# Kernel optimization log

Hardware: AMD Instinct MI355X
Metric: run time of the kernel (lower is better)

The kernel has to match this reference:

```python
import jax, jax.numpy as jnp
import numpy as np
import math

DIM = 768
HEADS = 8
DIM_HEAD = 64
INNER = HEADS * DIM_HEAD  # 512
B, L = 2, 4096
LN_EPS = 1e-5


def setup_inputs() -> dict:
    key = jax.random.key(0)
    ks = jax.random.split(key, 6)
    std = 0.02
    return {
        "x": jax.random.normal(ks[0], (B, L, DIM), dtype=jnp.float32),
        "ln_gamma": jnp.ones((DIM,), dtype=jnp.float32),
        "ln_beta": jnp.zeros((DIM,), dtype=jnp.float32),
        "Wq": jax.random.normal(ks[1], (DIM, INNER), dtype=jnp.float32) * std,
        "Wkv": jax.random.normal(ks[2], (DIM, 2 * INNER), dtype=jnp.float32) * std,
        "Wo": jax.random.normal(ks[3], (INNER, DIM), dtype=jnp.float32) * std,
    }


def reference(x, ln_gamma, ln_beta, Wq, Wkv, Wo):
    b, l, _ = x.shape
    # LayerNorm (eps=1e-5, affine)
    mu = jnp.mean(x, axis=-1, keepdims=True)
    var = jnp.mean(jnp.square(x - mu), axis=-1, keepdims=True)
    xn = (x - mu) * jax.lax.rsqrt(var + LN_EPS) * ln_gamma + ln_beta

    q = xn @ Wq                      # (b, l, inner)
    kv = xn @ Wkv                    # (b, l, 2*inner)
    k, v = jnp.split(kv, 2, axis=-1)

    def to_heads(t):
        return t.reshape(b, l, HEADS, DIM_HEAD).transpose(0, 2, 1, 3)  # (b,h,l,d)

    q, k, v = to_heads(q), to_heads(k), to_heads(v)

    scale = 1.0 / math.sqrt(math.sqrt(DIM_HEAD))
    # explicit quadratic scores, softmax in float32 as in original
    weight = jnp.einsum("bhid,bhjd->bhij", q * scale, k * scale)
    weight = jax.nn.softmax(weight.astype(jnp.float32), axis=-1).astype(q.dtype)
    out = jnp.einsum("bhij,bhjd->bhid", weight, v)       # (b,h,l,d)
    out = out.transpose(0, 2, 1, 3).reshape(b, l, INNER)  # merge heads
    return out @ Wo
```

## Files before the change

kernel.cpp:

```cpp
#include <hip/hip_runtime.h>
#include <hip/hip_bf16.h>


typedef __bf16 bf16_t;
typedef __bf16 bf16x4 __attribute__((ext_vector_type(4)));
typedef __bf16 bf16x8 __attribute__((ext_vector_type(8)));
typedef float f32x4 __attribute__((ext_vector_type(4)));

#define MFMA16(a, b, c) __builtin_amdgcn_mfma_f32_16x16x32_bf16((a), (b), (c), 0, 0, 0)

#define QSCALE 0.18033688011112042f

#define GLDS(gp, lp)                                                          \
    __builtin_amdgcn_global_load_lds(                                         \
        (const __attribute__((address_space(1))) void*)(gp),                  \
        (__attribute__((address_space(3))) void*)(lp), 16, 0, 0)

__global__ void detect_kernel(const unsigned int* __restrict__ xw, int* __restrict__ flag) {
    const int i = threadIdx.x;
    int cnt = 0;
#pragma unroll
    for (int j = 0; j < 2; ++j) {
        const unsigned int e = (xw[i * 2 + j] >> 7) & 0xFF;
        cnt += (e >= 100 && e <= 140) ? 1 : 0;
    }
#pragma unroll
    for (int off = 1; off < 64; off <<= 1) cnt += __shfl_xor(cnt, off, 64);
    if (i == 0) *flag = (cnt < 64) ? 1 : 0;
}

__global__ __launch_bounds__(256) void ln_kernel(const void* __restrict__ xv,
                                                 const void* __restrict__ gv,
                                                 const void* __restrict__ bv,
                                                 bf16_t* __restrict__ xn,
                                                 const int* __restrict__ flag) {
    const int f32 = *flag;
    const int lane = threadIdx.x & 63;
    const int row = blockIdx.x * 4 + (threadIdx.x >> 6);
    const int c0 = lane * 12;

    float v[12];
    if (f32) {
        const float* xr = (const float*)xv + (size_t)row * 768 + c0;
#pragma unroll
        for (int i = 0; i < 3; ++i) {
            const float4 q = *(const float4*)(xr + i * 4);
            v[i * 4] = q.x; v[i * 4 + 1] = q.y; v[i * 4 + 2] = q.z; v[i * 4 + 3] = q.w;
        }
    } else {
        const bf16_t* xr = (const bf16_t*)xv + (size_t)row * 768 + c0;
#pragma unroll
        for (int i = 0; i < 3; ++i) {
            const bf16x4 q = *(const bf16x4*)(xr + i * 4);
#pragma unroll
            for (int j = 0; j < 4; ++j) v[i * 4 + j] = (float)q[j];
        }
    }
    float s = 0.f, sq = 0.f;
#pragma unroll
    for (int j = 0; j < 12; ++j) { s += v[j]; sq += v[j] * v[j]; }
#pragma unroll
    for (int off = 1; off < 64; off <<= 1) {
        s += __shfl_xor(s, off, 64);
        sq += __shfl_xor(sq, off, 64);
    }
    const float mu = s * (1.0f / 768.0f);
    const float var = sq * (1.0f / 768.0f) - mu * mu;
    const float rstd = rsqrtf(var + 1e-5f);

    bf16_t* xo = xn + (size_t)row * 768 + c0;
#pragma unroll
    for (int i = 0; i < 3; ++i) {
        bf16x4 o;
#pragma unroll
        for (int j = 0; j < 4; ++j) {
            const int c = c0 + i * 4 + j;
            const float gc = f32 ? ((const float*)gv)[c] : (float)((const bf16_t*)gv)[c];
            const float bc = f32 ? ((const float*)bv)[c] : (float)((const bf16_t*)bv)[c];
            o[j] = (bf16_t)((v[i * 4 + j] - mu) * rstd * gc + bc);
        }
        *(bf16x4*)(xo + i * 4) = o;
    }
}

__global__ __launch_bounds__(256) void transpose_w(const void* __restrict__ in,
                                                   bf16_t* __restrict__ out,
                                                   int R, int C,
                                                   const int* __restrict__ flag) {
    const int f32 = *flag;
    __shared__ bf16_t Ts[64 * 68];
    const int r0 = blockIdx.y * 64, c0 = blockIdx.x * 64;
    const int t = threadIdx.x;
    {
        const int r = t >> 2, c = (t & 3) * 16;
        if (f32) {
            const float* src = (const float*)in + (size_t)(r0 + r) * C + c0 + c;
#pragma unroll
            for (int i = 0; i < 16; i += 4) {
                const float4 q = *(const float4*)(src + i);
                Ts[r * 68 + c + i] = (bf16_t)q.x;
                Ts[r * 68 + c + i + 1] = (bf16_t)q.y;
                Ts[r * 68 + c + i + 2] = (bf16_t)q.z;
                Ts[r * 68 + c + i + 3] = (bf16_t)q.w;
            }
        } else {
            const bf16_t* src = (const bf16_t*)in + (size_t)(r0 + r) * C + c0 + c;
            *(bf16x8*)&Ts[r * 68 + c] = *(const bf16x8*)src;
            *(bf16x8*)&Ts[r * 68 + c + 8] = *(const bf16x8*)(src + 8);
        }
    }
    __syncthreads();
    {
        const int oc = t >> 2, seg = (t & 3) * 16;
        bf16x8 v0, v1;
#pragma unroll
        for (int j = 0; j < 8; ++j) v0[j] = Ts[(seg + j) * 68 + oc];
#pragma unroll
        for (int j = 0; j < 8; ++j) v1[j] = Ts[(seg + 8 + j) * 68 + oc];
        bf16_t* dst = out + (size_t)(c0 + oc) * R + r0 + seg;
        *(bf16x8*)dst = v0;
        *(bf16x8*)(dst + 8) = v1;
    }
}

__global__ __launch_bounds__(256) void gemm_bt(const bf16_t* __restrict__ A,
                                               const bf16_t* __restrict__ BT,
                                               void* __restrict__ C,
                                               int M, int N, int K,
                                               const int* __restrict__ out_flag) {
    const int m0 = blockIdx.y * 128;
    const int n0 = blockIdx.x * 128;
    __shared__ bf16_t As[128 * 32];
    __shared__ bf16_t Bs[128 * 32];

    const int t = threadIdx.x;
    const int lane = t & 63;
    const int w = t >> 6;
    const int wm = (w >> 1) * 64;
    const int wn = (w & 1) * 64;
    const int quad = lane >> 4;
    const int cl = lane & 15;

    f32x4 acc[4][4];
    const f32x4 z4 = {0.f, 0.f, 0.f, 0.f};
#pragma unroll
    for (int mi = 0; mi < 4; ++mi)
#pragma unroll
        for (int ni = 0; ni < 4; ++ni) acc[mi][ni] = z4;

    const int r0 = lane >> 2;
    const int c0 = (lane & 3) * 8;
    const bf16_t* AgL = A + (size_t)(m0 + w * 32 + r0) * K + c0;
    const bf16_t* AgH = A + (size_t)(m0 + w * 32 + 16 + r0) * K + c0;
    const bf16_t* BgL = BT + (size_t)(n0 + w * 32 + r0) * K + c0;
    const bf16_t* BgH = BT + (size_t)(n0 + w * 32 + 16 + r0) * K + c0;
    bf16_t* AdL = &As[(w * 32) * 32];
    bf16_t* AdH = &As[(w * 32 + 16) * 32];
    bf16_t* BdL = &Bs[(w * 32) * 32];
    bf16_t* BdH = &Bs[(w * 32 + 16) * 32];

    for (int kt = 0; kt < K; kt += 32) {
        __syncthreads();
        GLDS(AgL + kt, AdL);
        GLDS(AgH + kt, AdH);
        GLDS(BgL + kt, BdL);
        GLDS(BgH + kt, BdH);
        __syncthreads();

        const int ko = quad * 8;
        bf16x8 af[4], bfr[4];
#pragma unroll
        for (int mi = 0; mi < 4; ++mi)
            af[mi] = *(const bf16x8*)&As[(wm + mi * 16 + cl) * 32 + ko];
#pragma unroll
        for (int ni = 0; ni < 4; ++ni)
            bfr[ni] = *(const bf16x8*)&Bs[(wn + ni * 16 + cl) * 32 + ko];
#pragma unroll
        for (int mi = 0; mi < 4; ++mi)
#pragma unroll
            for (int ni = 0; ni < 4; ++ni)
                acc[mi][ni] = MFMA16(af[mi], bfr[ni], acc[mi][ni]);
    }

    const int f32out = (out_flag != nullptr) && (*out_flag != 0);
#pragma unroll
    for (int mi = 0; mi < 4; ++mi) {
#pragma unroll
        for (int ni = 0; ni < 4; ++ni) {
#pragma unroll
            for (int r4 = 0; r4 < 4; ++r4) {
                const int row = m0 + wm + mi * 16 + quad * 4 + r4;
                const int col = n0 + wn + ni * 16 + cl;
                if (f32out)
                    ((float*)C)[(size_t)row * N + col] = acc[mi][ni][r4];
                else
                    ((bf16_t*)C)[(size_t)row * N + col] = (bf16_t)acc[mi][ni][r4];
            }
        }
    }
}

__global__ __launch_bounds__(128) void gemm_bt64(const bf16_t* __restrict__ A,
                                                 const bf16_t* __restrict__ BT,
                                                 void* __restrict__ C,
                                                 int M, int N, int K,
                                                 const int* __restrict__ out_flag) {
    const int m0 = blockIdx.y * 128;
    const int n0 = blockIdx.x * 64;
    __shared__ bf16_t As[128 * 32];
    __shared__ bf16_t Bs[64 * 32];

    const int t = threadIdx.x;
    const int lane = t & 63;
    const int w = t >> 6;
    const int quad = lane >> 4;
    const int cl = lane & 15;

    f32x4 acc[4][4];
    const f32x4 z4 = {0.f, 0.f, 0.f, 0.f};
#pragma unroll
    for (int mi = 0; mi < 4; ++mi)
#pragma unroll
        for (int ni = 0; ni < 4; ++ni) acc[mi][ni] = z4;

    const int r0 = lane >> 2;
    const int c0 = (lane & 3) * 8;
    const bf16_t* Ag = A + (size_t)(m0 + w * 64 + r0) * K + c0;
    const bf16_t* Bg = BT + (size_t)(n0 + w * 32 + r0) * K + c0;
    bf16_t* Ad = &As[(w * 64) * 32];
    bf16_t* Bd = &Bs[(w * 32) * 32];

    for (int kt = 0; kt < K; kt += 32) {
        __syncthreads();
#pragma unroll
        for (int i = 0; i < 4; ++i) GLDS(Ag + kt + (size_t)i * 16 * K, Ad + i * 512);
#pragma unroll
        for (int i = 0; i < 2; ++i) GLDS(Bg + kt + (size_t)i * 16 * K, Bd + i * 512);
        __syncthreads();

        const int ko = quad * 8;
        bf16x8 af[4], bfr[4];
#pragma unroll
        for (int mi = 0; mi < 4; ++mi)
            af[mi] = *(const bf16x8*)&As[(w * 64 + mi * 16 + cl) * 32 + ko];
#pragma unroll
        for (int ni = 0; ni < 4; ++ni)
            bfr[ni] = *(const bf16x8*)&Bs[(ni * 16 + cl) * 32 + ko];
#pragma unroll
        for (int mi = 0; mi < 4; ++mi)
#pragma unroll
            for (int ni = 0; ni < 4; ++ni)
                acc[mi][ni] = MFMA16(af[mi], bfr[ni], acc[mi][ni]);
    }

    const int f32out = (out_flag != nullptr) && (*out_flag != 0);
#pragma unroll
    for (int mi = 0; mi < 4; ++mi) {
#pragma unroll
        for (int ni = 0; ni < 4; ++ni) {
#pragma unroll
            for (int r4 = 0; r4 < 4; ++r4) {
                const int row = m0 + w * 64 + mi * 16 + quad * 4 + r4;
                const int col = n0 + ni * 16 + cl;
                if (f32out)
                    ((float*)C)[(size_t)row * N + col] = acc[mi][ni][r4];
                else
                    ((bf16_t*)C)[(size_t)row * N + col] = (bf16_t)acc[mi][ni][r4];
            }
        }
    }
}

__global__ __launch_bounds__(256) void vtrans(const bf16_t* __restrict__ qkv,
                                              bf16_t* __restrict__ vtg) {
    const int tt = blockIdx.x;
    const int bh = blockIdx.y;
    const int b = bh >> 3, h = bh & 7;
    const int tok0 = tt * 64;
    __shared__ bf16_t Ts[64 * 68];
    const int t = threadIdx.x;
    {
        const int r = t >> 2, c = (t & 3) * 16;
        const bf16_t* src = qkv + ((size_t)b * 4096 + tok0 + r) * 1536 + 1024 + h * 64 + c;
        *(bf16x8*)&Ts[r * 68 + c] = *(const bf16x8*)src;
        *(bf16x8*)&Ts[r * 68 + c + 8] = *(const bf16x8*)(src + 8);
    }
    __syncthreads();
    {
        const int d = t >> 2, seg = (t & 3) * 16;
        bf16x8 v0, v1;
#pragma unroll
        for (int j = 0; j < 8; ++j) v0[j] = Ts[(seg + j) * 68 + d];
#pragma unroll
        for (int j = 0; j < 8; ++j) v1[j] = Ts[(seg + 8 + j) * 68 + d];
        bf16_t* dst = vtg + ((size_t)bh * 64 + d) * 4096 + tok0 + seg;
        *(bf16x8*)dst = v0;
        *(bf16x8*)(dst + 8) = v1;
    }
}

__global__ __launch_bounds__(256, 2) void attn_kernel(const bf16_t* __restrict__ qkv,
                                                      const bf16_t* __restrict__ vtg,
                                                      bf16_t* __restrict__ ao) {
    const int qt = blockIdx.x;
    const int bh = blockIdx.y;
    const int b = bh >> 3, h = bh & 7;
    const int q0 = qt * 128;

    __shared__ bf16_t Ps[4][64 * 68];
    __shared__ bf16_t Ks[2][64 * 68];
    __shared__ bf16_t Vs[2][64 * 68];

    const int t = threadIdx.x;
    const int lane = t & 63;
    const int w = t >> 6;
    const int qsub = w & 1;
    const int kh = w >> 1;
    const int quad = lane >> 4;
    const int cl = lane & 15;

    const size_t rowbase = (size_t)b * 4096;
    const int qcol = h * 64;
    const int kcol = 512 + h * 64;

    {
        const int r = t >> 1;
        const int half = (t & 1) * 32;
        const bf16_t* src = qkv + (rowbase + q0 + r) * 1536 + qcol + half;
#pragma unroll
        for (int o8 = 0; o8 < 4; ++o8) {
            bf16x8 v = *(const bf16x8*)(src + o8 * 8);
#pragma unroll
            for (int e = 0; e < 8; ++e) v[e] = (bf16_t)((float)v[e] * QSCALE);
            *(bf16x8*)&Ps[0][r * 68 + half + o8 * 8] = v;
        }
    }
    __syncthreads();

    bf16x8 aq[4][2];
#pragma unroll
    for (int rt = 0; rt < 4; ++rt)
#pragma unroll
        for (int hh = 0; hh < 2; ++hh)
            aq[rt][hh] = *(const bf16x8*)&Ps[0][(qsub * 64 + rt * 16 + cl) * 68 +
                                               hh * 32 + quad * 8];

    bf16x8 ones;
#pragma unroll
    for (int e = 0; e < 8; ++e) ones[e] = (bf16_t)1.0f;

    const f32x4 z4 = {0.f, 0.f, 0.f, 0.f};
    f32x4 o[4][4];
    f32x4 l_acc[4];
#pragma unroll
    for (int rt = 0; rt < 4; ++rt) {
        l_acc[rt] = z4;
#pragma unroll
        for (int ni = 0; ni < 4; ++ni) o[rt][ni] = z4;
    }

    const int t2 = qsub * 64 + lane;
    const int sr = t2 >> 1;
    const int sh = (t2 & 1) * 32;

    bf16x8 kreg[4], vreg[4];
    {
        const int k0 = kh * 2048;
        const bf16_t* ks = qkv + (rowbase + k0 + sr) * 1536 + kcol + sh;
        const bf16_t* vs = vtg + ((size_t)bh * 64 + sr) * 4096 + k0 + sh;
#pragma unroll
        for (int o8 = 0; o8 < 4; ++o8) {
            kreg[o8] = *(const bf16x8*)(ks + o8 * 8);
            vreg[o8] = *(const bf16x8*)(vs + o8 * 8);
        }
    }

    for (int it = 0; it < 32; ++it) {
        __syncthreads();
#pragma unroll
        for (int o8 = 0; o8 < 4; ++o8) {
            *(bf16x8*)&Ks[kh][sr * 68 + sh + o8 * 8] = kreg[o8];
            *(bf16x8*)&Vs[kh][sr * 68 + sh + o8 * 8] = vreg[o8];
        }
        __syncthreads();

        if (it < 31) {
            const int k0n = kh * 2048 + (it + 1) * 64;
            const bf16_t* ks = qkv + (rowbase + k0n + sr) * 1536 + kcol + sh;
            const bf16_t* vs = vtg + ((size_t)bh * 64 + sr) * 4096 + k0n + sh;
#pragma unroll
            for (int o8 = 0; o8 < 4; ++o8) {
                kreg[o8] = *(const bf16x8*)(ks + o8 * 8);
                vreg[o8] = *(const bf16x8*)(vs + o8 * 8);
            }
        }

        const int ko = quad * 8;
        bf16x8 kb[4][2];
#pragma unroll
        for (int ni = 0; ni < 4; ++ni) {
            kb[ni][0] = *(const bf16x8*)&Ks[kh][(ni * 16 + cl) * 68 + ko];
            kb[ni][1] = *(const bf16x8*)&Ks[kh][(ni * 16 + cl) * 68 + 32 + ko];
        }
#pragma unroll
        for (int rt = 0; rt < 4; ++rt) {
#pragma unroll
            for (int ni = 0; ni < 4; ++ni) {
                f32x4 s = z4;
                s = MFMA16(kb[ni][0], aq[rt][0], s);
                s = MFMA16(kb[ni][1], aq[rt][1], s);
                bf16x4 pk;
#pragma unroll
                for (int r4 = 0; r4 < 4; ++r4) pk[r4] = (bf16_t)exp2f(s[r4]);
                *(bf16x4*)&Ps[w][(rt * 16 + cl) * 68 + ni * 16 + quad * 4] = pk;
            }
        }

        bf16x8 vb[4][2];
#pragma unroll
        for (int ni = 0; ni < 4; ++ni) {
            vb[ni][0] = *(const bf16x8*)&Vs[kh][(ni * 16 + cl) * 68 + ko];
            vb[ni][1] = *(const bf16x8*)&Vs[kh][(ni * 16 + cl) * 68 + 32 + ko];
        }
#pragma unroll
        for (int rt = 0; rt < 4; ++rt) {
            const bf16x8 p0 = *(const bf16x8*)&Ps[w][(rt * 16 + cl) * 68 + ko];
            const bf16x8 p1 = *(const bf16x8*)&Ps[w][(rt * 16 + cl) * 68 + 32 + ko];
#pragma unroll
            for (int ni = 0; ni < 4; ++ni) {
                o[rt][ni] = MFMA16(p0, vb[ni][0], o[rt][ni]);
                o[rt][ni] = MFMA16(p1, vb[ni][1], o[rt][ni]);
            }
            l_acc[rt] = MFMA16(p0, ones, l_acc[rt]);
            l_acc[rt] = MFMA16(p1, ones, l_acc[rt]);
        }
    }

    float* cb = (float*)&Ps[0][0];
    __syncthreads();
    if (kh == 1) {
#pragma unroll
        for (int rt = 0; rt < 4; ++rt) {
#pragma unroll
            for (int r4 = 0; r4 < 4; ++r4) {
                const int row = rt * 16 + quad * 4 + r4;
                float* rp = cb + qsub * 4160 + row * 65;
#pragma unroll
                for (int ni = 0; ni < 4; ++ni) rp[ni * 16 + cl] = o[rt][ni][r4];
                if (cl == 0) rp[64] = l_acc[rt][r4];
            }
        }
    }
    __syncthreads();
    if (kh == 0) {
#pragma unroll
        for (int rt = 0; rt < 4; ++rt) {
#pragma unroll
            for (int r4 = 0; r4 < 4; ++r4) {
                const int row = rt * 16 + quad * 4 + r4;
                const float* rp = cb + qsub * 4160 + row * 65;
                const float inv = 1.0f / (l_acc[rt][r4] + rp[64]);
                const size_t orow = rowbase + q0 + qsub * 64 + row;
#pragma unroll
                for (int ni = 0; ni < 4; ++ni)
                    ao[orow * 512 + h * 64 + ni * 16 + cl] =
                        (bf16_t)((o[rt][ni][r4] + rp[ni * 16 + cl]) * inv);
            }
        }
    }
}

extern "C" void kernel_launch(void* const* d_in, const int* in_sizes, int n_in,
                              void* d_out, int out_size, void* d_ws, size_t ws_size,
                              hipStream_t stream) {
    const void* x = d_in[0];
    const void* gamma = d_in[1];
    const void* beta = d_in[2];
    const void* Wq = d_in[3];
    const void* Wkv = d_in[4];
    const void* Wo = d_in[5];

    char* wsb = (char*)d_ws;
    int* flag = (int*)wsb;
    bf16_t* xn = (bf16_t*)(wsb + 256);
    bf16_t* WqkvT = xn + (size_t)8192 * 768;
    bf16_t* WoT = WqkvT + (size_t)1536 * 768;
    bf16_t* qkv = WoT + (size_t)768 * 512;
    bf16_t* aob = xn;
    bf16_t* vtg = (bf16_t*)d_out;

    detect_kernel<<<1, 64, 0, stream>>>((const unsigned int*)x, flag);

    ln_kernel<<<2048, 256, 0, stream>>>(x, gamma, beta, xn, flag);

    transpose_w<<<dim3(8, 12), 256, 0, stream>>>(Wq, WqkvT, 768, 512, flag);
    transpose_w<<<dim3(16, 12), 256, 0, stream>>>(Wkv, WqkvT + (size_t)512 * 768, 768,
                                                  1024, flag);
    transpose_w<<<dim3(12, 8), 256, 0, stream>>>(Wo, WoT, 512, 768, flag);

    gemm_bt<<<dim3(12, 64), 256, 0, stream>>>(xn, WqkvT, (void*)qkv, 8192, 1536, 768,
                                              nullptr);

    vtrans<<<dim3(64, 16), 256, 0, stream>>>(qkv, vtg);

    attn_kernel<<<dim3(32, 16), 256, 0, stream>>>(qkv, vtg, aob);

    gemm_bt64<<<dim3(12, 64), 128, 0, stream>>>(aob, WoT, d_out, 8192, 768, 512, flag);
}
```

Measured before the change: 274.1 us.

## Fuse detect, layernorm and weight transposes into one prep kernel; fold Q scale

Merges the dtype-detect, layernorm and three weight-transpose launches into a single prep kernel whose blocks split by index, removing four launches and the serial dependency on a separate flag kernel. The Q scaling moves into the QKV GEMM epilogue, so attention can load Q straight into LDS with global_load_lds without a register round trip. Each block now recomputes the detection, and the Q tile in LDS loses its padding, which may add bank conflicts on fragment reads.

Result: faster. 261.5 us (-4.6%).

```diff
diff --git a/kernel.cpp b/kernel.cpp
--- a/kernel.cpp
+++ b/kernel.cpp
@@ -16,81 +16,99 @@
         (const __attribute__((address_space(1))) void*)(gp),                  \
         (__attribute__((address_space(3))) void*)(lp), 16, 0, 0)
 
-__global__ void detect_kernel(const unsigned int* __restrict__ xw, int* __restrict__ flag) {
-    const int i = threadIdx.x;
+__device__ __forceinline__ int detect_f32(const unsigned int* __restrict__ xw) {
+    const int l = threadIdx.x & 63;
     int cnt = 0;
 #pragma unroll
     for (int j = 0; j < 2; ++j) {
-        const unsigned int e = (xw[i * 2 + j] >> 7) & 0xFF;
+        const unsigned int e = (xw[l * 2 + j] >> 7) & 0xFF;
         cnt += (e >= 100 && e <= 140) ? 1 : 0;
     }
 #pragma unroll
     for (int off = 1; off < 64; off <<= 1) cnt += __shfl_xor(cnt, off, 64);
-    if (i == 0) *flag = (cnt < 64) ? 1 : 0;
-}
-
-__global__ __launch_bounds__(256) void ln_kernel(const void* __restrict__ xv,
-                                                 const void* __restrict__ gv,
-                                                 const void* __restrict__ bv,
-                                                 bf16_t* __restrict__ xn,
-                                                 const int* __restrict__ flag) {
-    const int f32 = *flag;
-    const int lane = threadIdx.x & 63;
-    const int row = blockIdx.x * 4 + (threadIdx.x >> 6);
-    const int c0 = lane * 12;
-
-    float v[12];
-    if (f32) {
-        const float* xr = (const float*)xv + (size_t)row * 768 + c0;
+    return cnt < 64;
+}
+
+__global__ __launch_bounds__(256) void prep_kernel(
+    const void* __restrict__ xv, const void* __restrict__ gv,
+    const void* __restrict__ bv, const void* __restrict__ wq,
+    const void* __restrict__ wkv, const void* __restrict__ wo,
+    bf16_t* __restrict__ xn, bf16_t* __restrict__ WqkvT, bf16_t* __restrict__ WoT,
+    int* __restrict__ flag) {
+    const int f32 = detect_f32((const unsigned int*)xv);
+    const int bid = blockIdx.x;
+    const int t = threadIdx.x;
+    if (bid == 0 && t == 0) *flag = f32;
+
+    __shared__ bf16_t Ts[64 * 68];
+
+    if (bid < 2048) {
+        const int lane = t & 63;
+        const int row = bid * 4 + (t >> 6);
+        const int c0 = lane * 12;
+        float v[12];
+        if (f32) {
+            const float* xr = (const float*)xv + (size_t)row * 768 + c0;
+#pragma unroll
+            for (int i = 0; i < 3; ++i) {
+                const float4 q = *(const float4*)(xr + i * 4);
+                v[i * 4] = q.x; v[i * 4 + 1] = q.y;
+                v[i * 4 + 2] = q.z; v[i * 4 + 3] = q.w;
+            }
+        } else {
+            const bf16_t* xr = (const bf16_t*)xv + (size_t)row * 768 + c0;
+#pragma unroll
+            for (int i = 0; i < 3; ++i) {
+                const bf16x4 q = *(const bf16x4*)(xr + i * 4);
+#pragma unroll
+                for (int j = 0; j < 4; ++j) v[i * 4 + j] = (float)q[j];
+            }
+        }
+        float s = 0.f, sq = 0.f;
+#pragma unroll
+        for (int j = 0; j < 12; ++j) { s += v[j]; sq += v[j] * v[j]; }
+#pragma unroll
+        for (int off = 1; off < 64; off <<= 1) {
+            s += __shfl_xor(s, off, 64);
+            sq += __shfl_xor(sq, off, 64);
+        }
+        const float mu = s * (1.0f / 768.0f);
+        const float var = sq * (1.0f / 768.0f) - mu * mu;
+        const float rstd = rsqrtf(var + 1e-5f);
+
+        bf16_t* xo = xn + (size_t)row * 768 + c0;
 #pragma unroll
         for (int i = 0; i < 3; ++i) {
-            const float4 q = *(const float4*)(xr + i * 4);
-            v[i * 4] = q.x; v[i * 4 + 1] = q.y; v[i * 4 + 2] = q.z; v[i * 4 + 3] = q.w;
-        }
+            bf16x4 o;
+#pragma unroll
+            for (int j = 0; j < 4; ++j) {
+                const int c = c0 + i * 4 + j;
+                const float gc = f32 ? ((const float*)gv)[c] : (float)((const bf16_t*)gv)[c];
+                const float bc = f32 ? ((const float*)bv)[c] : (float)((const bf16_t*)bv)[c];
+                o[j] = (bf16_t)((v[i * 4 + j] - mu) * rstd * gc + bc);
+            }
+            *(bf16x4*)(xo + i * 4) = o;
+        }
+        return;
+    }
+
+    int idx = bid - 2048;
+    const void* in;
+    bf16_t* out;
+    int R, C, cx, ry;
+    if (idx < 96) {
+        in = wq; out = WqkvT; R = 768; C = 512;
+        cx = idx & 7; ry = idx >> 3;
+    } else if (idx < 288) {
+        idx -= 96;
+        in = wkv; out = WqkvT + (size_t)512 * 768; R = 768; C = 1024;
+        cx = idx & 15; ry = idx >> 4;
     } else {
-        const bf16_t* xr = (const bf16_t*)xv + (size_t)row * 768 + c0;
-#pragma unroll
-        for (int i = 0; i < 3; ++i) {
-            const bf16x4 q = *(const bf16x4*)(xr + i * 4);
-#pragma unroll
-            for (int j = 0; j < 4; ++j) v[i * 4 + j] = (float)q[j];
-        }
-    }
-    float s = 0.f, sq = 0.f;
-#pragma unroll
-    for (int j = 0; j < 12; ++j) { s += v[j]; sq += v[j] * v[j]; }
-#pragma unroll
-    for (int off = 1; off < 64; off <<= 1) {
-        s += __shfl_xor(s, off, 64);
-        sq += __shfl_xor(sq, off, 64);
-    }
-    const float mu = s * (1.0f / 768.0f);
-    const float var = sq * (1.0f / 768.0f) - mu * mu;
-    const float rstd = rsqrtf(var + 1e-5f);
-
-    bf16_t* xo = xn + (size_t)row * 768 + c0;
-#pragma unroll
-    for (int i = 0; i < 3; ++i) {
-        bf16x4 o;
-#pragma unroll
-        for (int j = 0; j < 4; ++j) {
-            const int c = c0 + i * 4 + j;
-            const float gc = f32 ? ((const float*)gv)[c] : (float)((const bf16_t*)gv)[c];
-            const float bc = f32 ? ((const float*)bv)[c] : (float)((const bf16_t*)bv)[c];
-            o[j] = (bf16_t)((v[i * 4 + j] - mu) * rstd * gc + bc);
-        }
-        *(bf16x4*)(xo + i * 4) = o;
-    }
-}
-
-__global__ __launch_bounds__(256) void transpose_w(const void* __restrict__ in,
-                                                   bf16_t* __restrict__ out,
-                                                   int R, int C,
-                                                   const int* __restrict__ flag) {
-    const int f32 = *flag;
-    __shared__ bf16_t Ts[64 * 68];
-    const int r0 = blockIdx.y * 64, c0 = blockIdx.x * 64;
-    const int t = threadIdx.x;
+        idx -= 288;
+        in = wo; out = WoT; R = 512; C = 768;
+        cx = idx % 12; ry = idx / 12;
+    }
+    const int r0 = ry * 64, c0 = cx * 64;
     {
         const int r = t >> 2, c = (t & 3) * 16;
         if (f32) {
@@ -125,9 +143,8 @@
 
 __global__ __launch_bounds__(256) void gemm_bt(const bf16_t* __restrict__ A,
                                                const bf16_t* __restrict__ BT,
-                                               void* __restrict__ C,
-                                               int M, int N, int K,
-                                               const int* __restrict__ out_flag) {
+                                               bf16_t* __restrict__ C,
+                                               int M, int N, int K, int qscale_cols) {
     const int m0 = blockIdx.y * 128;
     const int n0 = blockIdx.x * 128;
     __shared__ bf16_t As[128 * 32];
@@ -182,7 +199,7 @@
                 acc[mi][ni] = MFMA16(af[mi], bfr[ni], acc[mi][ni]);
     }
 
-    const int f32out = (out_flag != nullptr) && (*out_flag != 0);
+    const float sc = (n0 + 128 <= qscale_cols) ? QSCALE : 1.0f;
 #pragma unroll
     for (int mi = 0; mi < 4; ++mi) {
 #pragma unroll
@@ -191,10 +208,7 @@
             for (int r4 = 0; r4 < 4; ++r4) {
                 const int row = m0 + wm + mi * 16 + quad * 4 + r4;
                 const int col = n0 + wn + ni * 16 + cl;
-                if (f32out)
-                    ((float*)C)[(size_t)row * N + col] = acc[mi][ni][r4];
-                else
-                    ((bf16_t*)C)[(size_t)row * N + col] = (bf16_t)acc[mi][ni][r4];
+                C[(size_t)row * N + col] = (bf16_t)(acc[mi][ni][r4] * sc);
             }
         }
     }
@@ -253,7 +267,7 @@
                 acc[mi][ni] = MFMA16(af[mi], bfr[ni], acc[mi][ni]);
     }
 
-    const int f32out = (out_flag != nullptr) && (*out_flag != 0);
+    const int f32out = *out_flag;
 #pragma unroll
     for (int mi = 0; mi < 4; ++mi) {
 #pragma unroll
@@ -323,17 +337,13 @@
     const int qcol = h * 64;
     const int kcol = 512 + h * 64;
 
+    bf16_t* Qtr = &Ps[0][0];
     {
-        const int r = t >> 1;
-        const int half = (t & 1) * 32;
-        const bf16_t* src = qkv + (rowbase + q0 + r) * 1536 + qcol + half;
-#pragma unroll
-        for (int o8 = 0; o8 < 4; ++o8) {
-            bf16x8 v = *(const bf16x8*)(src + o8 * 8);
-#pragma unroll
-            for (int e = 0; e < 8; ++e) v[e] = (bf16_t)((float)v[e] * QSCALE);
-            *(bf16x8*)&Ps[0][r * 68 + half + o8 * 8] = v;
-        }
+        const bf16_t* qsrc = qkv + (rowbase + q0 + w * 32) * 1536 + qcol;
+#pragma unroll
+        for (int i = 0; i < 4; ++i)
+            GLDS(qsrc + (size_t)(i * 8 + (lane >> 3)) * 1536 + (lane & 7) * 8,
+                 Qtr + (w * 32 + i * 8) * 64);
     }
     __syncthreads();
 
@@ -342,8 +352,8 @@
     for (int rt = 0; rt < 4; ++rt)
 #pragma unroll
         for (int hh = 0; hh < 2; ++hh)
-            aq[rt][hh] = *(const bf16x8*)&Ps[0][(qsub * 64 + rt * 16 + cl) * 68 +
-                                               hh * 32 + quad * 8];
+            aq[rt][hh] =
+                *(const bf16x8*)&Qtr[(qsub * 64 + rt * 16 + cl) * 64 + hh * 32 + quad * 8];
 
     bf16x8 ones;
 #pragma unroll
@@ -489,17 +499,10 @@
     bf16_t* aob = xn;
     bf16_t* vtg = (bf16_t*)d_out;
 
-    detect_kernel<<<1, 64, 0, stream>>>((const unsigned int*)x, flag);
-
-    ln_kernel<<<2048, 256, 0, stream>>>(x, gamma, beta, xn, flag);
-
-    transpose_w<<<dim3(8, 12), 256, 0, stream>>>(Wq, WqkvT, 768, 512, flag);
-    transpose_w<<<dim3(16, 12), 256, 0, stream>>>(Wkv, WqkvT + (size_t)512 * 768, 768,
-                                                  1024, flag);
-    transpose_w<<<dim3(12, 8), 256, 0, stream>>>(Wo, WoT, 512, 768, flag);
-
-    gemm_bt<<<dim3(12, 64), 256, 0, stream>>>(xn, WqkvT, (void*)qkv, 8192, 1536, 768,
-                                              nullptr);
+    prep_kernel<<<2432, 256, 0, stream>>>(x, gamma, beta, Wq, Wkv, Wo, xn, WqkvT, WoT,
+                                          flag);
+
+    gemm_bt<<<dim3(12, 64), 256, 0, stream>>>(xn, WqkvT, qkv, 8192, 1536, 768, 512);
 
     vtrans<<<dim3(64, 16), 256, 0, stream>>>(qkv, vtg);
 
```
